# Optimization experiments

Hardware: AMD Instinct MI355X
Metric: run time of the kernel (lower is better)

Reference implementation:

```python
import jax, jax.numpy as jnp
from jax import lax
import numpy as np

B, S, IN = 8, 4096, 64
D, H, K = 512, 8, 3
TCN_CH = [256, 256, 512]
HD = D // H


def setup_inputs() -> dict:
    key = jax.random.key(0)
    ks = iter(jax.random.split(key, 64))
    def nrm(shape, s=0.02):
        return jax.random.normal(next(ks), shape, jnp.float32) * s
    inp = {"x": jax.random.normal(next(ks), (B, S, IN), jnp.float32)}
    inp["W_in"] = nrm((IN, D)); inp["b_in"] = jnp.zeros((D,), jnp.float32)
    chans = [D] + TCN_CH
    for i in range(3):
        cin, cout = chans[i], chans[i + 1]
        inp[f"c1w{i}"] = nrm((cout, cin, K), 0.01); inp[f"c1b{i}"] = jnp.zeros((cout,), jnp.float32)
        inp[f"c2w{i}"] = nrm((cout, cout, K), 0.01); inp[f"c2b{i}"] = jnp.zeros((cout,), jnp.float32)
        if cin != cout:  # downsample 1x1 conv (blocks 0 and 2)
            inp[f"dsw{i}"] = nrm((cout, cin, 1), 0.01); inp[f"dsb{i}"] = jnp.zeros((cout,), jnp.float32)
    inp["W_tcn"] = nrm((TCN_CH[-1], D)); inp["b_tcn"] = jnp.zeros((D,), jnp.float32)
    NL = 2  # attention layers, stacked on leading axis
    for n in ["Wq", "Wk", "Wv", "Wo"]:
        inp[n] = nrm((NL, D, D))
    for n in ["bq", "bk", "bv", "bo", "ln_b"]:
        inp[n] = jnp.zeros((NL, D), jnp.float32)
    inp["ln_g"] = jnp.ones((NL, D), jnp.float32)
    inp["W_out"] = nrm((D, 1)); inp["b_out"] = jnp.zeros((1,), jnp.float32)
    return inp


def _conv(x, w, b, dil, pad):
    # x: (B,C,L), w: (O,I,K)
    y = lax.conv_general_dilated(x, w, (1,), [(pad, pad)], rhs_dilation=(dil,),
                                 dimension_numbers=("NCH", "OIH", "NCH"))
    return y + b[None, :, None]


def _block(t, c1w, c1b, c2w, c2b, ds, dil):
    # TemporalConvBlock: symmetric padding (k-1)*dil on both convs, truncate to input length
    pad = (K - 1) * dil
    o = jax.nn.relu(_conv(t, c1w, c1b, dil, pad))   # length L + pad
    o = _conv(o, c2w, c2b, dil, pad)                # length L + 2*pad
    r = t if ds is None else _conv(t, ds[0], ds[1], 1, 0)
    return jax.nn.relu(o[:, :, : t.shape[2]] + r)


def _layernorm(x, g, b, eps=1e-5):
    mu = x.mean(-1, keepdims=True)
    var = ((x - mu) ** 2).mean(-1, keepdims=True)
    return (x - mu) * lax.rsqrt(var + eps) * g + b


def _forward(x, W_in, b_in, c1w0, c1b0, c2w0, c2b0, dsw0, dsb0,
             c1w1, c1b1, c2w1, c2b1, c1w2, c1b2, c2w2, c2b2, dsw2, dsb2,
             W_tcn, b_tcn, Wq, bq, Wk, bk, Wv, bv, Wo, bo, ln_g, ln_b, W_out, b_out):
    h = x @ W_in + b_in                              # (B,S,D)
    t = jnp.swapaxes(h, 1, 2)                        # (B,D,S)
    t = _block(t, c1w0, c1b0, c2w0, c2b0, (dsw0, dsb0), 1)
    t = _block(t, c1w1, c1b1, c2w1, c2b1, None, 2)
    t = _block(t, c1w2, c1b2, c2w2, c2b2, (dsw2, dsb2), 4)
    h = h + jnp.swapaxes(t, 1, 2) @ W_tcn + b_tcn
    # sinusoidal positional encoding
    pos = jnp.arange(S, dtype=jnp.float32)[:, None]
    div = jnp.exp(jnp.arange(0, D, 2, dtype=jnp.float32) * (-np.log(10000.0) / D))
    pe = jnp.stack([jnp.sin(pos * div), jnp.cos(pos * div)], axis=-1).reshape(S, D)
    h = h + pe[None]
    for l in range(Wq.shape[0]):
        res = h
        def heads(y):  # (B,S,D) -> (B,H,S,HD)
            return y.reshape(B, S, H, HD).transpose(0, 2, 1, 3)
        q = heads(h @ Wq[l] + bq[l])
        k = heads(h @ Wk[l] + bk[l])
        v = heads(h @ Wv[l] + bv[l])
        qf = jax.nn.elu(q) + 1.0
        kf = jax.nn.elu(k) + 1.0
        kv = jnp.einsum("bhnd,bhnm->bhdm", kf, v)            # (B,H,HD,HD)
        out = jnp.einsum("bhnd,bhdm->bhnm", qf, kv)          # (B,H,S,HD)
        norm = jnp.maximum(jnp.einsum("bhnd,bhd->bhn", qf, kf.sum(2)), 1e-6)
        out = out / norm[..., None]
        out = out.transpose(0, 2, 1, 3).reshape(B, S, D)
        h = _layernorm(res + out @ Wo[l] + bo[l], ln_g[l], ln_b[l])
    pooled = h.mean(1)                                       # (B,D)
    return (pooled @ W_out + b_out)[:, 0]                    # (B,)


def reference(x, W_in, b_in, c1w0, c1b0, c2w0, c2b0, dsw0, dsb0,
              c1w1, c1b1, c2w1, c2b1, c1w2, c1b2, c2w2, c2b2, dsw2, dsb2,
              W_tcn, b_tcn, Wq, bq, Wk, bk, Wv, bv, Wo, bo, ln_g, ln_b, W_out, b_out):
    return _forward(x, W_in, b_in, c1w0, c1b0, c2w0, c2b0, dsw0, dsb0,
                    c1w1, c1b1, c2w1, c2b1, c1w2, c1b2, c2w2, c2b2, dsw2, dsb2,
                    W_tcn, b_tcn, Wq, bq, Wk, bk, Wv, bv, Wo, bo, ln_g, ln_b, W_out, b_out)
```

## Files before the change

kernel.cpp:

```cpp
#include <hip/hip_runtime.h>

typedef unsigned short u16;
typedef unsigned int u32;
typedef short bhalf8 __attribute__((ext_vector_type(8)));
typedef float f32x4 __attribute__((ext_vector_type(4)));

#define S_LEN 4096
#define NSEG 30

__device__ __forceinline__ float b2f(u16 h){ return __uint_as_float(((u32)h) << 16); }
__device__ __forceinline__ u16 f2b(float f){
  u32 u = __float_as_uint(f);
  return (u16)((u + 0x7FFFu + ((u >> 16) & 1u)) >> 16);
}
__device__ __forceinline__ u32 cvtpk(float a, float b){
  u32 r; asm("v_cvt_pk_bf16_f32 %0, %1, %2" : "=v"(r) : "v"(a), "v"(b)); return r;
}
__device__ __forceinline__ void unp8(uint4 v, float* f){
  f[0]=__uint_as_float(v.x<<16); f[1]=__uint_as_float(v.x&0xffff0000u);
  f[2]=__uint_as_float(v.y<<16); f[3]=__uint_as_float(v.y&0xffff0000u);
  f[4]=__uint_as_float(v.z<<16); f[5]=__uint_as_float(v.z&0xffff0000u);
  f[6]=__uint_as_float(v.w<<16); f[7]=__uint_as_float(v.w&0xffff0000u);
}
__device__ __forceinline__ void unp4(uint2 v, float* f){
  f[0]=__uint_as_float(v.x<<16); f[1]=__uint_as_float(v.x&0xffff0000u);
  f[2]=__uint_as_float(v.y<<16); f[3]=__uint_as_float(v.y&0xffff0000u);
}

__device__ __forceinline__ size_t taddr(int r, int c, int C){
  return (size_t)(r >> 7) * ((size_t)C << 7) + (size_t)((c >> 5) << 12)
       + ((r & 127) << 5) + (c & 31);
}

__device__ __forceinline__ void gload16(const void* g, void* l){
  __builtin_amdgcn_global_load_lds(
      (__attribute__((address_space(1))) void*)(g),
      (__attribute__((address_space(3))) void*)(l), 16, 0, 0);
}

struct PrepArgs {
  const float* src[NSEG];
  int N[NSEG]; int K[NSEG]; int sn[NSEG]; int sk[NSEG]; unsigned off[NSEG];
};

__global__ __launch_bounds__(256) void prep_w(PrepArgs pa, u16* __restrict__ wb){
  int seg = blockIdx.y;
  int N = pa.N[seg], K = pa.K[seg];
  int ntk = (K + 31) >> 5;
  int tiles = ((N + 31) >> 5) * ntk;
  int tile = blockIdx.x;
  if (tile >= tiles) return;
  int n0 = (tile / ntk) << 5, k0 = (tile % ntk) << 5;
  const float* src = pa.src[seg];
  long sn = pa.sn[seg], sk = pa.sk[seg];
  u16* dst = wb + pa.off[seg];
  int lk = threadIdx.x & 31, ln = threadIdx.x >> 5;
  #pragma unroll
  for (int i = 0; i < 4; ++i){
    int n = n0 + ln + i*8, k = k0 + lk;
    if (n < N && k < K)
      dst[(size_t)n*K + k] = f2b(src[(long)n*sn + (long)k*sk]);
  }
}

__global__ __launch_bounds__(256) void pe_k(float* __restrict__ pe){
  int id = blockIdx.x*256 + threadIdx.x;
  int s = id >> 8, i = id & 255;
  float div = expf((float)i * (-2.0f * 9.210340371976184f / 512.0f));
  float a = (float)s * div;
  pe[(size_t)s*512 + 2*i]   = sinf(a);
  pe[(size_t)s*512 + 2*i+1] = cosf(a);
}

__global__ __launch_bounds__(256) void cvt_k(const float* __restrict__ x, u16* __restrict__ xb, int n){
  int id = blockIdx.x*256 + threadIdx.x;
  if (id < n){
    int r = id >> 6, c = id & 63;
    xb[taddr(r, c, 64)] = f2b(x[id]);
  }
}

template<int NTAPS, int KS1, int KS2>
__global__ __launch_bounds__(256) void gemm_k(
    const u16* __restrict__ A, const u16* __restrict__ W,
    const u16* __restrict__ A2, const u16* __restrict__ W2,
    const float* __restrict__ bias, const float* __restrict__ bias2,
    const float* __restrict__ bias3,
    u16* __restrict__ out, const u16* __restrict__ resb,
    const float* __restrict__ peb, const float* __restrict__ den,
    int N, int CA, int CA2, int dil, int nN, int wbstride, int flags)
{
  constexpr int DEPTH = (NTAPS == 1) ? 4 : 2;
  constexpr int AR    = (NTAPS == 1) ? 128 : 144;
  constexpr int HALO  = (NTAPS == 1) ? 0 : 8;
  constexpr int K     = KS1 << 5;
  constexpr int K2    = KS2 << 5;
  constexpr int TOTAL = KS1 + KS2;
  __shared__ u16 As[DEPTH][AR*32];
  __shared__ u16 Bs[DEPTH][NTAPS*128*32];
  const int tid = threadIdx.x;
  const int wave = tid >> 6, lane = tid & 63;
  const int wm = wave >> 1, wn = wave & 1;

  const int nwg = gridDim.x;
  const int lin = blockIdx.x;
  const int swz = (lin & 7) * (nwg >> 3) + (lin >> 3);
  const int mb = swz / nN, nb = swz - mb * nN;
  const int m0 = mb << 7, n0 = nb << 7;
  const bool bnd = (m0 & (S_LEN - 1)) == 0;

  const u16* Ae = (flags & 16) ? (A + (((size_t)(n0 & 511) >> 5) << 12)) : A;

  const int lr4 = lane >> 2, lc4 = lane & 3;
  const int c0 = lane >> 4, fro = lane & 15;

  const f32x4 zf = {0.f, 0.f, 0.f, 0.f};
  const bhalf8 zb = {0,0,0,0,0,0,0,0};
  f32x4 acc[4][4];
  #pragma unroll
  for (int i=0;i<4;++i)
    #pragma unroll
    for (int j=0;j<4;++j) acc[i][j] = zf;

  const u16* Wb = W + (size_t)(m0 >> 12) * (size_t)wbstride;
  const size_t abase  = (size_t)mb * ((size_t)CA  << 7);
  const size_t abase2 = (size_t)mb * ((size_t)CA2 << 7);

  auto STAGE = [&](int s, int b){
    if (s < KS1){
      const size_t tb = abase + ((size_t)s << 12);
      #pragma unroll
      for (int half = 0; half < 2; ++half){
        int mrow = (wave << 5) + (half << 4) + lr4;
        int i = mrow + HALO;
        int cg = lc4 ^ ((i >> 1) & 3);
        gload16(Ae + tb + mrow*32 + (cg << 3), &As[b][(HALO + (wave << 5) + (half << 4)) * 32]);
      }
      if (NTAPS > 1 && wave == 0 && lane < 32){
        int j = lr4;
        int cg = lc4 ^ ((j >> 1) & 3);
        size_t hb_ = (mb ? abase - ((size_t)CA << 7) : abase) + ((size_t)s << 12) + (120 + j)*32;
        gload16(Ae + hb_ + (cg << 3), &As[b][0]);
      }
      const int kb = s << 5;
      #pragma unroll
      for (int tp = 0; tp < NTAPS; ++tp){
        const u16* Wt = Wb + (size_t)tp * N * K;
        #pragma unroll
        for (int half = 0; half < 2; ++half){
          int i = (wave << 5) + (half << 4) + lr4;
          int cg = lc4 ^ ((i >> 1) & 3);
          gload16(Wt + (size_t)(n0 + i) * K + kb + (cg << 3),
                  &Bs[b][tp * 4096 + ((wave << 5) + (half << 4)) * 32]);
        }
      }
    } else if (KS2 > 0){
      const int t2 = s - KS1;
      const size_t tb = abase2 + ((size_t)t2 << 12);
      const int kb = t2 << 5;
      #pragma unroll
      for (int half = 0; half < 2; ++half){
        int mrow = (wave << 5) + (half << 4) + lr4;
        int i = mrow + HALO;
        int cg = lc4 ^ ((i >> 1) & 3);
        gload16(A2 + tb + mrow*32 + (cg << 3), &As[b][(HALO + (wave << 5) + (half << 4)) * 32]);
        int iB = (wave << 5) + (half << 4) + lr4;
        int cgB = lc4 ^ ((iB >> 1) & 3);
        gload16(W2 + (size_t)(n0 + iB) * K2 + kb + (cgB << 3),
                &Bs[b][((wave << 5) + (half << 4)) * 32]);
      }
    }
  };

  auto COMPUTE = [&](int s, int b){
    if (s < KS1){
      #pragma unroll
      for (int tp = 0; tp < NTAPS; ++tp){
        const int sh = (tp - NTAPS + 1) * dil;
        bhalf8 af[4], bf[4];
        #pragma unroll
        for (int mt = 0; mt < 4; ++mt){
          int r8 = (wm << 6) + (mt << 4) + fro + HALO + sh;
          af[mt] = *(const bhalf8*)&As[b][r8 * 32 + ((c0 ^ ((r8 >> 1) & 3)) << 3)];
        }
        if (NTAPS > 1 && bnd && wm == 0 && fro + sh < 0) af[0] = zb;
        #pragma unroll
        for (int nt = 0; nt < 4; ++nt){
          int rB = (wn << 6) + (nt << 4) + fro;
          bf[nt] = *(const bhalf8*)&Bs[b][tp * 4096 + rB * 32 + ((c0 ^ ((rB >> 1) & 3)) << 3)];
        }
        #pragma unroll
        for (int mt = 0; mt < 4; ++mt)
          #pragma unroll
          for (int nt = 0; nt < 4; ++nt)
            acc[mt][nt] = __builtin_amdgcn_mfma_f32_16x16x32_bf16(bf[nt], af[mt], acc[mt][nt], 0, 0, 0);
      }
    } else if (KS2 > 0){
      bhalf8 af[4], bf[4];
      #pragma unroll
      for (int mt = 0; mt < 4; ++mt){
        int r8 = (wm << 6) + (mt << 4) + fro + HALO;
        af[mt] = *(const bhalf8*)&As[b][r8 * 32 + ((c0 ^ ((r8 >> 1) & 3)) << 3)];
      }
      #pragma unroll
      for (int nt = 0; nt < 4; ++nt){
        int rB = (wn << 6) + (nt << 4) + fro;
        bf[nt] = *(const bhalf8*)&Bs[b][rB * 32 + ((c0 ^ ((rB >> 1) & 3)) << 3)];
      }
      #pragma unroll
      for (int mt = 0; mt < 4; ++mt)
        #pragma unroll
        for (int nt = 0; nt < 4; ++nt)
          acc[mt][nt] = __builtin_amdgcn_mfma_f32_16x16x32_bf16(bf[nt], af[mt], acc[mt][nt], 0, 0, 0);
    }
  };

  if constexpr (NTAPS == 1){
    STAGE(0, 0);
    if constexpr (TOTAL > 1) STAGE(1, 1);
    if constexpr (TOTAL > 2) STAGE(2, 2);
    #pragma unroll
    for (int s = 0; s < TOTAL; ++s){
      if (s + 1 >= TOTAL)      asm volatile("s_waitcnt vmcnt(0)" ::: "memory");
      else if (s + 2 >= TOTAL) asm volatile("s_waitcnt vmcnt(4)" ::: "memory");
      else                     asm volatile("s_waitcnt vmcnt(8)" ::: "memory");
      __builtin_amdgcn_sched_barrier(0);
      __builtin_amdgcn_s_barrier();
      __builtin_amdgcn_sched_barrier(0);
      if (s + 3 < TOTAL) STAGE(s + 3, (s + 3) & 3);
      COMPUTE(s, s & 3);
    }
  } else {
    STAGE(0, 0);
    #pragma unroll
    for (int s = 0; s < TOTAL; ++s){
      __syncthreads();
      if (s + 1 < TOTAL) STAGE(s + 1, (s + 1) & 1);
      COMPUTE(s, s & 1);
    }
  }

  const int mb_l = (wm << 6) + fro;
  const int cb_l = (wn << 6) + (c0 << 2);
  const int th = n0 >> 9;
  #pragma unroll
  for (int mt = 0; mt < 4; ++mt){
    const int row = m0 + mb_l + (mt << 4);
    const size_t prow = (size_t)(row & (S_LEN - 1)) * 512;
    #pragma unroll
    for (int nt = 0; nt < 4; ++nt){
      const int col = n0 + cb_l + (nt << 4);
      float v0 = acc[mt][nt][0], v1 = acc[mt][nt][1], v2 = acc[mt][nt][2], v3 = acc[mt][nt][3];
      if (flags & 32){
        const float* bp = (th == 0) ? bias : ((th == 1) ? bias2 : bias3);
        if (bp){ float4 b4 = *(const float4*)&bp[col & 511]; v0+=b4.x; v1+=b4.y; v2+=b4.z; v3+=b4.w; }
      } else {
        if (bias) { float4 b4 = *(const float4*)&bias[col];  v0+=b4.x; v1+=b4.y; v2+=b4.z; v3+=b4.w; }
        if (bias2){ float4 b4 = *(const float4*)&bias2[col]; v0+=b4.x; v1+=b4.y; v2+=b4.z; v3+=b4.w; }
      }
      if (flags & 4){
        uint2 rv = *(const uint2*)(resb + taddr(row, col, N));
        float rf[4]; unp4(rv, rf);
        v0 += rf[0]; v1 += rf[1]; v2 += rf[2]; v3 += rf[3];
      }
      if (flags & 8){
        float4 p4 = *(const float4*)&peb[prow + col];
        v0 += p4.x; v1 += p4.y; v2 += p4.z; v3 += p4.w;
      }
      if (flags & 16){
        float d = fmaxf(den[((size_t)row << 3) + (col >> 6)], 1e-6f);
        float rd = 1.0f / d;
        v0 *= rd; v1 *= rd; v2 *= rd; v3 *= rd;
      }
      if (flags & 1){
        v0 = fmaxf(v0, 0.f); v1 = fmaxf(v1, 0.f); v2 = fmaxf(v2, 0.f); v3 = fmaxf(v3, 0.f);
      }
      if ((flags & 2) && (!(flags & 32) || th < 2)){
        v0 = (v0 > 0.f) ? (v0 + 1.f) : __expf(v0);
        v1 = (v1 > 0.f) ? (v1 + 1.f) : __expf(v1);
        v2 = (v2 > 0.f) ? (v2 + 1.f) : __expf(v2);
        v3 = (v3 > 0.f) ? (v3 + 1.f) : __expf(v3);
      }
      uint2 pk; pk.x = cvtpk(v0, v1); pk.y = cvtpk(v2, v3);
      *(uint2*)(out + taddr(row, col, N)) = pk;
    }
  }
}

__global__ __launch_bounds__(256) void kv_partial(
    const u16* __restrict__ qkv,
    float* __restrict__ kvp, float* __restrict__ ksp)
{
  const int bh = blockIdx.x;
  const int b = bh >> 3, h = bh & 7;
  const int ch = blockIdx.y;
  const int t = threadIdx.x;
  __shared__ u16 kfs[16][64];
  __shared__ u16 vs[16][64];
  float acc[4][4] = {{0.f}};
  float ks[4] = {0.f,0.f,0.f,0.f};
  const int d0 = (t >> 4) << 2;
  const int c0 = (t & 15) << 2;
  const int lr = t >> 4, lc = (t & 15) << 2;
  const int rowbase = (b << 12) + (ch << 9);
  const int ck = 512 + (h << 6) + lc;
  const int cv = 1024 + (h << 6) + lc;
  for (int g = 0; g < 32; ++g){
    int r = rowbase + (g << 4) + lr;
    *(uint2*)&kfs[lr][lc] = *(const uint2*)(qkv + taddr(r, ck, 1536));
    *(uint2*)&vs[lr][lc]  = *(const uint2*)(qkv + taddr(r, cv, 1536));
    __syncthreads();
    #pragma unroll
    for (int i = 0; i < 16; ++i){
      float kv4[4], vv4[4];
      unp4(*(const uint2*)&kfs[i][d0], kv4);
      unp4(*(const uint2*)&vs[i][c0], vv4);
      #pragma unroll
      for (int j=0;j<4;++j)
        #pragma unroll
        for (int k2=0;k2<4;++k2) acc[j][k2] += kv4[j]*vv4[k2];
      if ((t & 15) == 0){
        #pragma unroll
        for (int j=0;j<4;++j) ks[j] += kv4[j];
      }
    }
    __syncthreads();
  }
  float* dst = kvp + ((size_t)(bh << 3) + ch) * 4096;
  #pragma unroll
  for (int j=0;j<4;++j)
    #pragma unroll
    for (int k2=0;k2<4;++k2) dst[(d0+j)*64 + (c0+k2)] = acc[j][k2];
  if ((t & 15) == 0){
    float* kd = ksp + ((size_t)(bh << 3) + ch) * 64;
    #pragma unroll
    for (int j=0;j<4;++j) kd[d0+j] = ks[j];
  }
}

__global__ __launch_bounds__(256) void kvred_k(
    const float* __restrict__ kvp, const float* __restrict__ ksp,
    float* __restrict__ kvf, float* __restrict__ ksf)
{
  int bh = blockIdx.x, t = threadIdx.x;
  for (int e = t; e < 4096; e += 256){
    float s = 0.f;
    #pragma unroll
    for (int ch = 0; ch < 8; ++ch) s += kvp[((size_t)(bh<<3)+ch)*4096 + e];
    kvf[(size_t)bh*4096 + e] = s;
  }
  if (t < 64){
    float s = 0.f;
    #pragma unroll
    for (int ch = 0; ch < 8; ++ch) s += ksp[((size_t)(bh<<3)+ch)*64 + t];
    ksf[bh*64 + t] = s;
  }
}

__global__ __launch_bounds__(256) void den_k(const u16* __restrict__ qkv,
    const float* __restrict__ ksf, float* __restrict__ den)
{
  int id = blockIdx.x*256 + threadIdx.x;
  int r = id >> 3, h = id & 7;
  int b = r >> 12;
  const float* ks = ksf + ((b<<3)+h)*64;
  float s = 0.f;
  for (int d = 0; d < 64; d += 8){
    uint4 vq = *(const uint4*)(qkv + taddr(r, (h << 6) + d, 1536));
    float f[8]; unp8(vq, f);
    #pragma unroll
    for (int j=0;j<8;++j) s += f[j]*ks[d+j];
  }
  den[id] = s;
}

__global__ __launch_bounds__(256) void packkv2_k(const float* __restrict__ kvf, u16* __restrict__ wbd){
  int id = blockIdx.x*256 + threadIdx.x;
  int b = id >> 16;
  int n = (id >> 7) & 511, j = id & 127;
  float v = 0.f;
  if ((j >> 6) == ((n >> 6) & 1))
    v = kvf[((size_t)((b<<3)+(n>>6)))*4096 + (j & 63)*64 + (n & 63)];
  wbd[id] = f2b(v);
}

__global__ __launch_bounds__(256) void ln_k(const u16* __restrict__ in,
    const float* __restrict__ g, const float* __restrict__ beta, u16* __restrict__ out)
{
  int wave = threadIdx.x >> 6, lane = threadIdx.x & 63;
  int row = blockIdx.x*4 + wave;
  size_t ad = taddr(row, lane*8, 512);
  uint4 pv = *(const uint4*)(in + ad);
  float f[8]; unp8(pv, f);
  float s = 0.f, ss = 0.f;
  #pragma unroll
  for (int i=0;i<8;++i){ s += f[i]; ss += f[i]*f[i]; }
  for (int m=1;m<64;m<<=1){ s += __shfl_xor(s,m); ss += __shfl_xor(ss,m); }
  float mean = s * (1.f/512.f);
  float var = ss * (1.f/512.f) - mean*mean;
  float rstd = rsqrtf(fmaxf(var, 0.f) + 1e-5f);
  u16 o[8];
  #pragma unroll
  for (int i=0;i<8;++i){
    int c = lane*8 + i;
    o[i] = f2b((f[i]-mean)*rstd*g[c] + beta[c]);
  }
  *(uint4*)(out + ad) = *(uint4*)o;
}

__global__ __launch_bounds__(256) void pool1_k(const u16* __restrict__ hb,
    const float* __restrict__ wout, float* __restrict__ part)
{
  int b = blockIdx.x >> 6, ch = blockIdx.x & 63;
  int t = threadIdx.x;
  __shared__ float ws[512];
  for (int i=t;i<512;i+=256) ws[i] = wout[i];
  __syncthreads();
  int r = (b << 12) + (ch << 6) + (t >> 2);
  int c0 = (t & 3) << 7;
  float s = 0.f;
  for (int i=0;i<128;i+=8){
    uint4 v = *(const uint4*)(hb + taddr(r, c0 + i, 512));
    float f[8]; unp8(v, f);
    #pragma unroll
    for (int j=0;j<8;++j) s += f[j]*ws[c0+i+j];
  }
  __shared__ float red[256];
  red[t] = s; __syncthreads();
  for (int k=128;k;k>>=1){ if (t<k) red[t]+=red[t+k]; __syncthreads(); }
  if (!t) part[blockIdx.x] = red[0];
}

__global__ __launch_bounds__(64) void pool2_k(const float* __restrict__ part,
    const float* __restrict__ bout, float* __restrict__ out)
{
  int b = blockIdx.x, t = threadIdx.x;
  float s = part[(b << 6) + t];
  for (int m=1;m<64;m<<=1) s += __shfl_xor(s,m);
  if (!t) out[b] = s * (1.f/4096.f) + bout[0];
}

extern "C" void kernel_launch(void* const* d_in, const int* in_sizes, int n_in,
                              void* d_out, int out_size, void* d_ws, size_t ws_size,
                              hipStream_t stream)
{
  (void)in_sizes; (void)n_in; (void)out_size; (void)ws_size;
  const float* x    = (const float*)d_in[0];
  const float* W_in = (const float*)d_in[1];
  const float* b_in = (const float*)d_in[2];
  const float* c1w0 = (const float*)d_in[3];
  const float* c1b0 = (const float*)d_in[4];
  const float* c2w0 = (const float*)d_in[5];
  const float* c2b0 = (const float*)d_in[6];
  const float* dsw0 = (const float*)d_in[7];
  const float* dsb0 = (const float*)d_in[8];
  const float* c1w1 = (const float*)d_in[9];
  const float* c1b1 = (const float*)d_in[10];
  const float* c2w1 = (const float*)d_in[11];
  const float* c2b1 = (const float*)d_in[12];
  const float* c1w2 = (const float*)d_in[13];
  const float* c1b2 = (const float*)d_in[14];
  const float* c2w2 = (const float*)d_in[15];
  const float* c2b2 = (const float*)d_in[16];
  const float* dsw2 = (const float*)d_in[17];
  const float* dsb2 = (const float*)d_in[18];
  const float* W_tcn= (const float*)d_in[19];
  const float* b_tcn= (const float*)d_in[20];
  const float* Wq   = (const float*)d_in[21];
  const float* Wk   = (const float*)d_in[22];
  const float* Wv   = (const float*)d_in[23];
  const float* Wo   = (const float*)d_in[24];
  const float* bq   = (const float*)d_in[25];
  const float* bk   = (const float*)d_in[26];
  const float* bv   = (const float*)d_in[27];
  const float* bo   = (const float*)d_in[28];
  const float* lnb  = (const float*)d_in[29];
  const float* lng  = (const float*)d_in[30];
  const float* W_out= (const float*)d_in[31];
  const float* b_out= (const float*)d_in[32];

  char* base = (char*)d_ws;
  size_t off = 0;
  auto alloc = [&](size_t bytes) -> void* {
    void* p = base + off;
    off += (bytes + 255) & ~(size_t)255;
    return p;
  };
  u16* WB   = (u16*)alloc(4816896ull*2);
  u16* wbd  = (u16*)alloc(8ull*512*128*2);
  float* peb= (float*)alloc(4096ull*512*4);
  float* den= (float*)alloc(32768ull*8*4);
  float* kvp= (float*)alloc(512ull*4096*4);
  float* ksp= (float*)alloc(512ull*64*4);
  float* kvf= (float*)alloc(64ull*4096*4);
  float* ksf= (float*)alloc(64ull*64*4);
  float* part=(float*)alloc(512*4);
  u16* hb   = (u16*)alloc(32768ull*512*2);
  char* qkvR= (char*)alloc(32768ull*1536*2);
  u16* atto = (u16*)alloc(32768ull*512*2);

  u16* qkvb = (u16*)qkvR;
  u16* xb   = (u16*)(qkvR);
  u16* t1b  = (u16*)(qkvR + 4194304);
  u16* t2b  = (u16*)(qkvR + 20971520);
  u16* t3b  = (u16*)(qkvR + 37748736);
  u16* o1b  = atto;

  unsigned wo_ = 0;
  auto wseg = [&](unsigned e){ unsigned o = wo_; wo_ += e; return o; };
  unsigned oWin  = wseg(512*64);
  unsigned oC1w0 = wseg(3*256*512);
  unsigned oC2w0 = wseg(3*256*256);
  unsigned oDs0  = wseg(256*512);
  unsigned oC1w1 = wseg(3*256*256);
  unsigned oC2w1 = wseg(3*256*256);
  unsigned oC1w2 = wseg(3*512*256);
  unsigned oC2w2 = wseg(3*512*512);
  unsigned oDs2  = wseg(512*256);
  unsigned oWtcn = wseg(512*512);
  unsigned oQKV  = wseg(2*1536*512);
  unsigned oWo   = wseg(2*512*512);

  PrepArgs pa;
  int si = 0;
  auto seg = [&](const float* s, int N, int K, int sn, int sk, unsigned o){
    pa.src[si]=s; pa.N[si]=N; pa.K[si]=K; pa.sn[si]=sn; pa.sk[si]=sk; pa.off[si]=o; ++si;
  };
  seg(W_in, 512, 64, 1, 512, oWin);
  for (int t=0;t<3;++t) seg(c1w0 + t, 256, 512, 1536, 3, oC1w0 + t*131072);
  for (int t=0;t<3;++t) seg(c2w0 + t, 256, 256,  768, 3, oC2w0 + t*65536);
  seg(dsw0, 256, 512, 512, 1, oDs0);
  for (int t=0;t<3;++t) seg(c1w1 + t, 256, 256,  768, 3, oC1w1 + t*65536);
  for (int t=0;t<3;++t) seg(c2w1 + t, 256, 256,  768, 3, oC2w1 + t*65536);
  for (int t=0;t<3;++t) seg(c1w2 + t, 512, 256,  768, 3, oC1w2 + t*131072);
  for (int t=0;t<3;++t) seg(c2w2 + t, 512, 512, 1536, 3, oC2w2 + t*262144);
  seg(dsw2, 512, 256, 256, 1, oDs2);
  seg(W_tcn, 512, 512, 1, 512, oWtcn);
  for (int l=0;l<2;++l){
    seg(Wq + l*262144, 512, 512, 1, 512, oQKV + l*786432 + 0);
    seg(Wk + l*262144, 512, 512, 1, 512, oQKV + l*786432 + 262144);
    seg(Wv + l*262144, 512, 512, 1, 512, oQKV + l*786432 + 524288);
  }
  for (int l=0;l<2;++l) seg(Wo + l*262144, 512, 512, 1, 512, oWo + l*262144);

  prep_w<<<dim3(256, NSEG), 256, 0, stream>>>(pa, WB);
  pe_k<<<4096, 256, 0, stream>>>(peb);
  cvt_k<<<8192, 256, 0, stream>>>(x, xb, 32768*64);

  const int RELU=1, ELU1=2, RES=4, PE=8, DIV=16, QKV=32;
  auto gemm = [&](const u16* A, const u16* W, const u16* A2, const u16* W2,
                  const float* b1, const float* b2, const float* b3,
                  u16* out, const u16* resb,
                  int K, int K2, int N, int CA, int CA2, int ntaps,
                  int dil, int wbs, int flags){
    int nN = N >> 7;
    dim3 grid(256 * nN);
    if (ntaps == 3){
      if (K == 512 && K2 == 0)
        gemm_k<3,16,0><<<grid, 256, 0, stream>>>(A, W, A2, W2, b1, b2, b3, out, resb,
                                                 peb, den, N, CA, CA2, dil, nN, wbs, flags);
      else if (K == 256 && K2 == 512)
        gemm_k<3,8,16><<<grid, 256, 0, stream>>>(A, W, A2, W2, b1, b2, b3, out, resb,
                                                 peb, den, N, CA, CA2, dil, nN, wbs, flags);
      else if (K == 256 && K2 == 0)
        gemm_k<3,8,0><<<grid, 256, 0, stream>>>(A, W, A2, W2, b1, b2, b3, out, resb,
                                                peb, den, N, CA, CA2, dil, nN, wbs, flags);
      else
        gemm_k<3,16,8><<<grid, 256, 0, stream>>>(A, W, A2, W2, b1, b2, b3, out, resb,
                                                 peb, den, N, CA, CA2, dil, nN, wbs, flags);
    } else {
      if (K == 64)
        gemm_k<1,2,0><<<grid, 256, 0, stream>>>(A, W, A2, W2, b1, b2, b3, out, resb,
                                                peb, den, N, CA, CA2, dil, nN, wbs, flags);
      else if (K == 128)
        gemm_k<1,4,0><<<grid, 256, 0, stream>>>(A, W, A2, W2, b1, b2, b3, out, resb,
                                                peb, den, N, CA, CA2, dil, nN, wbs, flags);
      else
        gemm_k<1,16,0><<<grid, 256, 0, stream>>>(A, W, A2, W2, b1, b2, b3, out, resb,
                                                 peb, den, N, CA, CA2, dil, nN, wbs, flags);
    }
  };

  gemm(xb, WB + oWin, nullptr, nullptr, b_in, nullptr, nullptr, hb, nullptr,
       64, 0, 512, 64, 0, 1, 1, 0, 0);
  gemm(hb,  WB + oC1w0, nullptr, nullptr, c1b0, nullptr, nullptr, o1b, nullptr,
       512, 0, 256, 512, 0, 3, 1, 0, RELU);
  gemm(o1b, WB + oC2w0, hb, WB + oDs0, c2b0, dsb0, nullptr, t1b, nullptr,
       256, 512, 256, 256, 512, 3, 1, 0, RELU);
  gemm(t1b, WB + oC1w1, nullptr, nullptr, c1b1, nullptr, nullptr, o1b, nullptr,
       256, 0, 256, 256, 0, 3, 2, 0, RELU);
  gemm(o1b, WB + oC2w1, nullptr, nullptr, c2b1, nullptr, nullptr, t2b, t1b,
       256, 0, 256, 256, 0, 3, 2, 0, RELU|RES);
  gemm(t2b, WB + oC1w2, nullptr, nullptr, c1b2, nullptr, nullptr, o1b, nullptr,
       256, 0, 512, 256, 0, 3, 4, 0, RELU);
  gemm(o1b, WB + oC2w2, t2b, WB + oDs2, c2b2, dsb2, nullptr, t3b, nullptr,
       512, 256, 512, 512, 256, 3, 4, 0, RELU);
  gemm(t3b, WB + oWtcn, nullptr, nullptr, b_tcn, nullptr, nullptr, hb, hb,
       512, 0, 512, 512, 0, 1, 1, 0, RES|PE);

  for (int l = 0; l < 2; ++l){
    gemm(hb, WB + oQKV + l*786432, nullptr, nullptr, bq + l*512, bk + l*512, bv + l*512,
         qkvb, nullptr, 512, 0, 1536, 512, 0, 1, 1, 0, ELU1|QKV);
    kv_partial<<<dim3(64, 8), 256, 0, stream>>>(qkvb, kvp, ksp);
    kvred_k<<<64, 256, 0, stream>>>(kvp, ksp, kvf, ksf);
    den_k<<<1024, 256, 0, stream>>>(qkvb, ksf, den);
    packkv2_k<<<2048, 256, 0, stream>>>(kvf, wbd);
    gemm(qkvb, wbd, nullptr, nullptr, nullptr, nullptr, nullptr, atto, nullptr,
         128, 0, 512, 1536, 0, 1, 1, 512*128, DIV);
    gemm(atto, WB + oWo + l*262144, nullptr, nullptr, bo + l*512, nullptr, nullptr, hb, hb,
         512, 0, 512, 512, 0, 1, 1, 0, RES);
    ln_k<<<8192, 256, 0, stream>>>(hb, lng + l*512, lnb + l*512, hb);
  }

  pool1_k<<<512, 256, 0, stream>>>(hb, W_out, part);
  pool2_k<<<8, 64, 0, stream>>>(part, b_out, (float*)d_out);
}
```

Measured before the change: 831.3 us.

## Pipeline 3-tap conv GEMM per tap with 4-deep weight buffers

The dilated 3-tap conv GEMM now splits each k-step into three per-tap stages. The A tile is loaded once per k-step and reused across the three taps, while weight tiles rotate through a 4-deep LDS ring. The old double-buffered loop with __syncthreads is replaced by the same vmcnt-counted, three-stage-ahead prefetch schedule the 1x1 path already used. This cuts LDS for the weight buffers from 2x3 tiles to 4 tiles and is meant to hide global-load latency better. The cost is more barriers per k-step and wait counts that rely on the load count per stage.

```diff
diff --git a/kernel.cpp b/kernel.cpp
--- a/kernel.cpp
+++ b/kernel.cpp
@@ -90,14 +90,15 @@
     const float* __restrict__ peb, const float* __restrict__ den,
     int N, int CA, int CA2, int dil, int nN, int wbstride, int flags)
 {
-  constexpr int DEPTH = (NTAPS == 1) ? 4 : 2;
-  constexpr int AR    = (NTAPS == 1) ? 128 : 144;
-  constexpr int HALO  = (NTAPS == 1) ? 0 : 8;
+  constexpr bool MT   = (NTAPS == 3);
+  constexpr int HALO  = MT ? 8 : 0;
+  constexpr int AR    = MT ? 144 : 128;
+  constexpr int DA    = (!MT) ? 4 : ((KS2 > 0) ? 4 : 2);
   constexpr int K     = KS1 << 5;
   constexpr int K2    = KS2 << 5;
-  constexpr int TOTAL = KS1 + KS2;
-  __shared__ u16 As[DEPTH][AR*32];
-  __shared__ u16 Bs[DEPTH][NTAPS*128*32];
+  constexpr int TOTAL = MT ? (3*KS1 + KS2) : (KS1 + KS2);
+  __shared__ u16 As[DA][AR*32];
+  __shared__ u16 Bs[4][128*32];
   const int tid = threadIdx.x;
   const int wave = tid >> 6, lane = tid & 63;
   const int wm = wave >> 1, wn = wave & 1;
@@ -126,99 +127,70 @@
   const size_t abase  = (size_t)mb * ((size_t)CA  << 7);
   const size_t abase2 = (size_t)mb * ((size_t)CA2 << 7);
 
-  auto STAGE = [&](int s, int b){
-    if (s < KS1){
-      const size_t tb = abase + ((size_t)s << 12);
+  auto STAGE_A = [&](int kb, int ab){
+    const size_t tb = abase + ((size_t)kb << 12);
+    #pragma unroll
+    for (int half = 0; half < 2; ++half){
+      int mrow = (wave << 5) + (half << 4) + lr4;
+      int i = mrow + HALO;
+      int cg = lc4 ^ ((i >> 1) & 3);
+      gload16(Ae + tb + mrow*32 + (cg << 3), &As[ab][(HALO + (wave << 5) + (half << 4)) * 32]);
+    }
+    if (MT && wave == 0 && lane < 32){
+      int j = lr4;
+      int cg = lc4 ^ ((j >> 1) & 3);
+      size_t hb_ = (mb ? abase - ((size_t)CA << 7) : abase) + ((size_t)kb << 12) + (120 + j)*32;
+      gload16(Ae + hb_ + (cg << 3), &As[ab][0]);
+    }
+  };
+  auto STAGE_A2 = [&](int t2, int ab){
+    const size_t tb = abase2 + ((size_t)t2 << 12);
+    #pragma unroll
+    for (int half = 0; half < 2; ++half){
+      int mrow = (wave << 5) + (half << 4) + lr4;
+      int i = mrow + HALO;
+      int cg = lc4 ^ ((i >> 1) & 3);
+      gload16(A2 + tb + mrow*32 + (cg << 3), &As[ab][(HALO + (wave << 5) + (half << 4)) * 32]);
+    }
+  };
+  auto STAGE_B = [&](const u16* Wt, size_t kstride, int kb, int bb){
+    #pragma unroll
+    for (int half = 0; half < 2; ++half){
+      int i = (wave << 5) + (half << 4) + lr4;
+      int cg = lc4 ^ ((i >> 1) & 3);
+      gload16(Wt + (size_t)(n0 + i) * kstride + (kb << 5) + (cg << 3),
+              &Bs[bb][((wave << 5) + (half << 4)) * 32]);
+    }
+  };
+  auto DO16 = [&](int ab, int bb, int sh, bool mask){
+    bhalf8 af[4], bf[4];
+    #pragma unroll
+    for (int mt = 0; mt < 4; ++mt){
+      int r8 = (wm << 6) + (mt << 4) + fro + HALO + sh;
+      af[mt] = *(const bhalf8*)&As[ab][r8 * 32 + ((c0 ^ ((r8 >> 1) & 3)) << 3)];
+    }
+    if (MT && mask && bnd && wm == 0 && fro + sh < 0) af[0] = zb;
+    #pragma unroll
+    for (int nt = 0; nt < 4; ++nt){
+      int rB = (wn << 6) + (nt << 4) + fro;
+      bf[nt] = *(const bhalf8*)&Bs[bb][rB * 32 + ((c0 ^ ((rB >> 1) & 3)) << 3)];
+    }
+    #pragma unroll
+    for (int mt = 0; mt < 4; ++mt)
       #pragma unroll
-      for (int half = 0; half < 2; ++half){
-        int mrow = (wave << 5) + (half << 4) + lr4;
-        int i = mrow + HALO;
-        int cg = lc4 ^ ((i >> 1) & 3);
-        gload16(Ae + tb + mrow*32 + (cg << 3), &As[b][(HALO + (wave << 5) + (half << 4)) * 32]);
-      }
-      if (NTAPS > 1 && wave == 0 && lane < 32){
-        int j = lr4;
-        int cg = lc4 ^ ((j >> 1) & 3);
-        size_t hb_ = (mb ? abase - ((size_t)CA << 7) : abase) + ((size_t)s << 12) + (120 + j)*32;
-        gload16(Ae + hb_ + (cg << 3), &As[b][0]);
-      }
-      const int kb = s << 5;
-      #pragma unroll
-      for (int tp = 0; tp < NTAPS; ++tp){
-        const u16* Wt = Wb + (size_t)tp * N * K;
-        #pragma unroll
-        for (int half = 0; half < 2; ++half){
-          int i = (wave << 5) + (half << 4) + lr4;
-          int cg = lc4 ^ ((i >> 1) & 3);
-          gload16(Wt + (size_t)(n0 + i) * K + kb + (cg << 3),
-                  &Bs[b][tp * 4096 + ((wave << 5) + (half << 4)) * 32]);
-        }
-      }
-    } else if (KS2 > 0){
-      const int t2 = s - KS1;
-      const size_t tb = abase2 + ((size_t)t2 << 12);
-      const int kb = t2 << 5;
-      #pragma unroll
-      for (int half = 0; half < 2; ++half){
-        int mrow = (wave << 5) + (half << 4) + lr4;
-        int i = mrow + HALO;
-        int cg = lc4 ^ ((i >> 1) & 3);
-        gload16(A2 + tb + mrow*32 + (cg << 3), &As[b][(HALO + (wave << 5) + (half << 4)) * 32]);
-        int iB = (wave << 5) + (half << 4) + lr4;
-        int cgB = lc4 ^ ((iB >> 1) & 3);
-        gload16(W2 + (size_t)(n0 + iB) * K2 + kb + (cgB << 3),
-                &Bs[b][((wave << 5) + (half << 4)) * 32]);
-      }
-    }
+      for (int nt = 0; nt < 4; ++nt)
+        acc[mt][nt] = __builtin_amdgcn_mfma_f32_16x16x32_bf16(bf[nt], af[mt], acc[mt][nt], 0, 0, 0);
   };
 
-  auto COMPUTE = [&](int s, int b){
-    if (s < KS1){
-      #pragma unroll
-      for (int tp = 0; tp < NTAPS; ++tp){
-        const int sh = (tp - NTAPS + 1) * dil;
-        bhalf8 af[4], bf[4];
-        #pragma unroll
-        for (int mt = 0; mt < 4; ++mt){
-          int r8 = (wm << 6) + (mt << 4) + fro + HALO + sh;
-          af[mt] = *(const bhalf8*)&As[b][r8 * 32 + ((c0 ^ ((r8 >> 1) & 3)) << 3)];
-        }
-        if (NTAPS > 1 && bnd && wm == 0 && fro + sh < 0) af[0] = zb;
-        #pragma unroll
-        for (int nt = 0; nt < 4; ++nt){
-          int rB = (wn << 6) + (nt << 4) + fro;
-          bf[nt] = *(const bhalf8*)&Bs[b][tp * 4096 + rB * 32 + ((c0 ^ ((rB >> 1) & 3)) << 3)];
-        }
-        #pragma unroll
-        for (int mt = 0; mt < 4; ++mt)
-          #pragma unroll
-          for (int nt = 0; nt < 4; ++nt)
-            acc[mt][nt] = __builtin_amdgcn_mfma_f32_16x16x32_bf16(bf[nt], af[mt], acc[mt][nt], 0, 0, 0);
-      }
-    } else if (KS2 > 0){
-      bhalf8 af[4], bf[4];
-      #pragma unroll
-      for (int mt = 0; mt < 4; ++mt){
-        int r8 = (wm << 6) + (mt << 4) + fro + HALO;
-        af[mt] = *(const bhalf8*)&As[b][r8 * 32 + ((c0 ^ ((r8 >> 1) & 3)) << 3)];
-      }
-      #pragma unroll
-      for (int nt = 0; nt < 4; ++nt){
-        int rB = (wn << 6) + (nt << 4) + fro;
-        bf[nt] = *(const bhalf8*)&Bs[b][rB * 32 + ((c0 ^ ((rB >> 1) & 3)) << 3)];
-      }
-      #pragma unroll
-      for (int mt = 0; mt < 4; ++mt)
-        #pragma unroll
-        for (int nt = 0; nt < 4; ++nt)
-          acc[mt][nt] = __builtin_amdgcn_mfma_f32_16x16x32_bf16(bf[nt], af[mt], acc[mt][nt], 0, 0, 0);
-    }
-  };
-
-  if constexpr (NTAPS == 1){
-    STAGE(0, 0);
-    if constexpr (TOTAL > 1) STAGE(1, 1);
-    if constexpr (TOTAL > 2) STAGE(2, 2);
+  if constexpr (!MT){
+    auto STG = [&](int s){
+      int b = s & 3;
+      if (s < KS1){ STAGE_A(s, b); STAGE_B(Wb, (size_t)K, s, b); }
+      else if (KS2 > 0){ STAGE_A2(s - KS1, b); STAGE_B(W2, (size_t)K2, s - KS1, b); }
+    };
+    STG(0);
+    if constexpr (TOTAL > 1) STG(1);
+    if constexpr (TOTAL > 2) STG(2);
     #pragma unroll
     for (int s = 0; s < TOTAL; ++s){
       if (s + 1 >= TOTAL)      asm volatile("s_waitcnt vmcnt(0)" ::: "memory");
@@ -227,16 +199,35 @@
       __builtin_amdgcn_sched_barrier(0);
       __builtin_amdgcn_s_barrier();
       __builtin_amdgcn_sched_barrier(0);
-      if (s + 3 < TOTAL) STAGE(s + 3, (s + 3) & 3);
-      COMPUTE(s, s & 3);
+      if (s + 3 < TOTAL) STG(s + 3);
+      DO16(s & 3, s & 3, 0, false);
     }
   } else {
-    STAGE(0, 0);
+    auto STG = [&](int s){
+      if (s < 3*KS1){
+        int kb = s / 3, tap = s % 3;
+        if (tap == 0) STAGE_A(kb, kb & (DA-1));
+        STAGE_B(Wb + (size_t)tap * N * K, (size_t)K, kb, s & 3);
+      } else if (KS2 > 0){
+        int t2 = s - 3*KS1;
+        STAGE_A2(t2, (KS1 + t2) & (DA-1));
+        STAGE_B(W2, (size_t)K2, t2, s & 3);
+      }
+    };
+    STG(0);
+    if constexpr (TOTAL > 1) STG(1);
+    if constexpr (TOTAL > 2) STG(2);
     #pragma unroll
     for (int s = 0; s < TOTAL; ++s){
-      __syncthreads();
-      if (s + 1 < TOTAL) STAGE(s + 1, (s + 1) & 1);
-      COMPUTE(s, s & 1);
+      if (s + 1 >= TOTAL)      asm volatile("s_waitcnt vmcnt(0)" ::: "memory");
+      else if (s + 2 >= TOTAL) asm volatile("s_waitcnt vmcnt(2)" ::: "memory");
+      else                     asm volatile("s_waitcnt vmcnt(4)" ::: "memory");
+      __builtin_amdgcn_sched_barrier(0);
+      __builtin_amdgcn_s_barrier();
+      __builtin_amdgcn_sched_barrier(0);
+      if (s + 3 < TOTAL) STG(s + 3);
+      if (s < 3*KS1) DO16((s/3) & (DA-1), s & 3, ((s%3) - 2) * dil, true);
+      else           DO16((KS1 + (s - 3*KS1)) & (DA-1), s & 3, 0, false);
     }
   }
 
```

Result: no change. 832.2 us (+0.1%).
